# Optimization experiments

Hardware: AMD Instinct MI355X
Metric: run time of the kernel (lower is better)

The kernel has to match this reference:

```python
import jax, jax.numpy as jnp
import numpy as np

NLAT_IN, NLON_IN = 360, 720
NLAT_OUT, NLON_OUT = 180, 360
KERNEL_SIZE = 3
THETA_CUTOFF = KERNEL_SIZE * np.pi / NLAT_IN  # default theta_cutoff
B, C = 2, 64


def _cc_lats_weights(n):
    # Clenshaw-Curtis quadrature on [-1,1] (torch-harmonics 'equiangular' grid);
    # latitudes (colatitude) = arccos(nodes) = pi*k/(n-1) in [0, pi].
    N = n - 1
    theta = np.pi * np.arange(n) / N
    w = np.ones(n)
    for j in range(1, N // 2 + 1):
        b = 1.0 if 2 * j == N else 2.0
        w -= b * np.cos(2.0 * j * theta) / (4.0 * j * j - 1.0)
    w *= 2.0 / N
    w[0] *= 0.5
    w[-1] *= 0.5
    return theta, w


def _precompute_psi():
    # Mirrors _precompute_convolution_tensor + _compute_support_vals_isotropic.
    d_theta = THETA_CUTOFF / KERNEL_SIZE
    lats_in, _ = _cc_lats_weights(NLAT_IN)
    lats_out, _ = _cc_lats_weights(NLAT_OUT)
    phis = np.linspace(0.0, 2.0 * np.pi, NLON_IN)
    alpha = -lats_in[None, :, None].astype(np.float32)   # [1, H, 1]
    beta = phis[None, None, :].astype(np.float32)        # [1, 1, W]
    gamma = lats_out[:, None, None].astype(np.float32)   # [T, 1, 1]
    z = np.cos(alpha) * np.cos(gamma) - np.cos(beta) * np.sin(alpha) * np.sin(gamma)
    with np.errstate(invalid="ignore"):
        theta = np.arccos(z)  # [T, H, W]; nan where |z|>1 (excluded by mask, as in torch)
    segs, lats, lons, vals = [], [], [], []
    for ik in range(KERNEL_SIZE):
        itheta = ik * d_theta
        with np.errstate(invalid="ignore"):
            mask = (np.abs(theta - itheta) < d_theta) & (theta < THETA_CUTOFF)
        t_idx, h_idx, w_idx = np.nonzero(mask)
        segs.append(ik * NLAT_OUT + t_idx)  # fused (kernel, nlat_out) segment id
        lats.append(h_idx)
        lons.append(w_idx)
        vals.append(1.0 - np.abs(theta[mask] - itheta) / d_theta)
    return (np.concatenate(segs).astype(np.int32),
            np.concatenate(lats).astype(np.int32),
            np.concatenate(lons).astype(np.int32),
            np.concatenate(vals).astype(np.float32))


def setup_inputs() -> dict:
    key = jax.random.key(0)
    x = jax.random.normal(key, (B, C, NLAT_IN, NLON_IN), dtype=jnp.float32)
    _, wgl = _cc_lats_weights(NLAT_IN)
    quad_weights = jnp.asarray(2.0 * np.pi * wgl[:, None] / NLON_IN, dtype=jnp.float32)
    seg, lat, lon, val = _precompute_psi()
    return {"x": x, "quad_weights": quad_weights,
            "psi_seg": jnp.asarray(seg), "psi_lat": jnp.asarray(lat),
            "psi_lon": jnp.asarray(lon), "psi_val": jnp.asarray(val)}


def reference(x, quad_weights, psi_seg, psi_lat, psi_lon, psi_val):
    # out[b,c,k,t,p] = sum_{(k,t,h,w) in psi} val * qw[h] * x[b,c,h,(w-(p+1)*s) mod W]
    Bx, Cx, H, W = x.shape
    scale = W // NLON_OUT  # longitudinal shift per output longitude (torch.roll step)
    xw = (quad_weights * x).reshape(Bx * Cx, H, W)  # [BC, H, W]
    num_seg = KERNEL_SIZE * NLAT_OUT

    def step(carry, p):
        cols = (psi_lon - (p + 1) * scale) % W                 # rolled longitude per nnz
        g = xw[:, psi_lat, cols] * psi_val                     # [BC, nnz] gather + scale
        out_p = jax.ops.segment_sum(g.T, psi_seg, num_segments=num_seg)  # [K*T, BC]
        return carry, out_p

    _, ys = jax.lax.scan(step, None, jnp.arange(NLON_OUT))     # [P, K*T, BC]
    out = ys.transpose(2, 1, 0).reshape(Bx, Cx, KERNEL_SIZE, NLAT_OUT, NLON_OUT)
    return out
```

## Files before the change

kernel.cpp:

```cpp
#include <hip/hip_runtime.h>


#define NLAT_IN  360
#define NLON_IN  720
#define NLAT_OUT 180
#define NLON_OUT 360
#define KSIZE    3
#define NSEG     (KSIZE * NLAT_OUT)
#define CHW      (NLAT_IN * NLON_IN)
#define BCTOT    128
#define G        4
#define NBCG     (BCTOT / G)
#define MAXR     2
#define PH       10
#define NTHREADS 256
#define SLOTS    432
#define MIRROR   (SLOTS - NLON_OUT)
#define ROWB     (SLOTS * 16)

typedef float v2f __attribute__((ext_vector_type(2)));

__device__ __forceinline__ void PKF(v2f& a, v2f x, v2f c) {
    asm("v_pk_fma_f32 %0, %1, %2, %0" : "+v"(a) : "v"(x), "v"(c));
}


__global__ void prep1_kernel(const int* __restrict__ seg, const int* __restrict__ lat,
                             const float* __restrict__ val, int nnz,
                             int* __restrict__ ptrh, int* __restrict__ hbase,
                             int* __restrict__ hlast, int* __restrict__ flags) {
    int idx = blockIdx.x * blockDim.x + threadIdx.x;
    if (idx >= NSEG * PH) return;
    int s = idx / PH, j = idx - s * PH;
    int lo = 0, hi = nnz;
    while (lo < hi) { int m = (lo + hi) >> 1; if (seg[m] < s) lo = m + 1; else hi = m; }
    int e0 = lo;
    lo = e0; hi = nnz;
    while (lo < hi) { int m = (lo + hi) >> 1; if (seg[m] < s + 1) lo = m + 1; else hi = m; }
    int e1 = lo;
    if (e0 >= e1) {
        ptrh[idx] = e0; flags[idx] = 0;
        if (j == 0) { hbase[s] = 1 << 28; hlast[s] = -(1 << 28); }
        return;
    }
    int hb = lat[e0];
    if (j == 0) { hbase[s] = hb; hlast[s] = lat[e1 - 1]; }
    int a;
    { int tg = hb + j; lo = e0; hi = e1;
      while (lo < hi) { int m = (lo + hi) >> 1; if (lat[m] < tg) lo = m + 1; else hi = m; }
      a = lo; }
    ptrh[idx] = a;
    int f = 0;
    if (j < PH - 1) {
        int tg = hb + j + 1; lo = a; hi = e1;
        while (lo < hi) { int m = (lo + hi) >> 1; if (lat[m] < tg) lo = m + 1; else hi = m; }
        int b = lo;
        if (b - a == NLON_IN) {
            float v0 = val[a], v1 = val[a + 240], v2 = val[a + 480];
            float d = fmaxf(fabsf(v0 - v1), fmaxf(fabsf(v0 - v2), fabsf(v1 - v2)));
            f = (d < 1e-5f) ? 1 : 0;
        }
    }
    flags[idx] = f;
}

__global__ void span_kernel(const int* __restrict__ hbase, const int* __restrict__ hlast,
                            int* __restrict__ hbU, int* __restrict__ hlU) {
    int t = blockIdx.x * blockDim.x + threadIdx.x;
    if (t >= NLAT_OUT) return;
    int lo = 1 << 28, hi = -(1 << 28);
#pragma unroll
    for (int k = 0; k < KSIZE; ++k) {
        lo = min(lo, hbase[k * NLAT_OUT + t]);
        hi = max(hi, hlast[k * NLAT_OUT + t]);
    }
    hbU[t] = lo; hlU[t] = hi;
}

__global__ void cf_kernel(const int* __restrict__ lat, const float* __restrict__ val,
                          const float* __restrict__ qw, int nnz, float* __restrict__ cfb) {
    int e = blockIdx.x * blockDim.x + threadIdx.x;
    if (e < nnz) cfb[e] = val[e] * qw[lat[e]];
}

__global__ void runs_kernel(const int* __restrict__ lon, const int* __restrict__ ptrh,
                            const int* __restrict__ flags,
                            int* __restrict__ runcnt, uint2* __restrict__ runslab) {
    const int idx  = blockIdx.x * 4 + (threadIdx.x >> 6);
    if (idx >= NSEG * PH) return;
    const int lane = threadIdx.x & 63;
    const int j = idx % PH;
    int runbase = 0;
    if (j < PH - 1) {
        const int a = ptrh[idx], b = ptrh[idx + 1];
        if (b > a && !flags[idx]) {
            for (int c = a; c < b; c += 64) {
                const int e = c + lane;
                const bool active = e < b;
                const int w   = active ? lon[e] : 0;
                const int wm1 = (active && e > a) ? lon[e - 1] : -99;
                const bool isStart = active && (lane == 0 || w != wm1 + 1);
                const unsigned long long mask = __ballot(isStart);
                if (isStart) {
                    const int cnt = min(64, b - c);
                    unsigned long long hv = (mask >> lane) >> 1;
                    const int len = hv ? __ffsll((long long)hv) : (cnt - lane);
                    const int cidx = __popcll(mask & ((1ull << lane) - 1ull));
                    const int s0 = ((w >> 1) + NLON_OUT - 1) % NLON_OUT;
                    runslab[a + runbase + cidx] = make_uint2(
                        (unsigned)e, (unsigned)(s0 | ((w & 1) << 9) | (len << 11)));
                }
                runbase += __popcll(mask);
            }
        }
    }
    if (lane == 0) runcnt[idx] = runbase;
}


__global__ __launch_bounds__(NTHREADS) void disco_kernel(
    const float* __restrict__ x,
    const float* __restrict__ cfb,
    const uint2* __restrict__ runslab,
    const int*   __restrict__ runcnt,
    const int*   __restrict__ ptrh,
    const int*   __restrict__ hbase,
    const int*   __restrict__ flags,
    const int*   __restrict__ hbU,
    const int*   __restrict__ hlU,
    float*       __restrict__ out)
{
    __shared__ float4 smem4[MAXR * 2 * SLOTS];
    float4 (*ldsx)[SLOTS] = (float4(*)[SLOTS])smem4;
    v2f    (*accbuf)[6]   = (v2f(*)[6])smem4;

    const int tid      = threadIdx.x;
    const int lane     = tid & 63;
    const int wpair    = tid >> 7;
    const int pairlane = tid & 127;
    const int pid      = (pairlane < 120) ? pairlane : pairlane - 120;
    const int p0       = 3 * pid;
    const int bc0      = blockIdx.x * G;
    const int ty       = blockIdx.y;
    const int t        = (ty & 1) ? (NLAT_OUT - 1 - (ty >> 1)) : (ty >> 1);

    const int rlo = hbU[t], rhi = hlU[t];
    const int hbK0 = hbase[t];
    const int hbK1 = hbase[NLAT_OUT + t];
    const int hbK2 = hbase[2 * NLAT_OUT + t];

    v2f acc[KSIZE][6] = {};
    const char* lb = (const char*)smem4;

    float2 sv0[4], sv1[4], sv2[4];
    const float* xb = x + (size_t)bc0 * CHW;

#define LOADW(R0)                                                              \
    {                                                                          \
        {   const int idx_ = tid;                                              \
            const int rr_ = idx_ >= 360;                                       \
            const int m_  = idx_ - 360 * rr_;                                  \
            const int row_ = min((R0) + rr_, rhi);                             \
            const float* xr_ = xb + (size_t)row_ * NLON_IN + 2 * m_;           \
            sv0[0] = *(const float2*)(xr_);                                    \
            sv0[1] = *(const float2*)(xr_ + CHW);                              \
            sv0[2] = *(const float2*)(xr_ + 2 * CHW);                          \
            sv0[3] = *(const float2*)(xr_ + 3 * CHW);                          \
        }                                                                      \
        {   const int idx_ = tid + 256;                                        \
            const int rr_ = idx_ >= 360;                                       \
            const int m_  = idx_ - 360 * rr_;                                  \
            const int row_ = min((R0) + rr_, rhi);                             \
            const float* xr_ = xb + (size_t)row_ * NLON_IN + 2 * m_;           \
            sv1[0] = *(const float2*)(xr_);                                    \
            sv1[1] = *(const float2*)(xr_ + CHW);                              \
            sv1[2] = *(const float2*)(xr_ + 2 * CHW);                          \
            sv1[3] = *(const float2*)(xr_ + 3 * CHW);                          \
        }                                                                      \
        if (tid < 208) {                                                       \
            const int m_  = tid + 512 - 360;                                   \
            const int row_ = min((R0) + 1, rhi);                               \
            const float* xr_ = xb + (size_t)row_ * NLON_IN + 2 * m_;           \
            sv2[0] = *(const float2*)(xr_);                                    \
            sv2[1] = *(const float2*)(xr_ + CHW);                              \
            sv2[2] = *(const float2*)(xr_ + 2 * CHW);                          \
            sv2[3] = *(const float2*)(xr_ + 3 * CHW);                          \
        }                                                                      \
    }

#define WRITEW()                                                               \
    {                                                                          \
        {   const int idx_ = tid;                                              \
            const int rr_ = idx_ >= 360;                                       \
            const int m_  = idx_ - 360 * rr_;                                  \
            const float4 ev_ = {sv0[0].x, sv0[1].x, sv0[2].x, sv0[3].x};       \
            const float4 ov_ = {sv0[0].y, sv0[1].y, sv0[2].y, sv0[3].y};       \
            ldsx[2 * rr_ + 0][m_] = ev_;                                       \
            ldsx[2 * rr_ + 1][m_] = ov_;                                       \
            if (m_ < MIRROR) {                                                 \
                ldsx[2 * rr_ + 0][NLON_OUT + m_] = ev_;                        \
                ldsx[2 * rr_ + 1][NLON_OUT + m_] = ov_;                        \
            }                                                                  \
        }                                                                      \
        {   const int idx_ = tid + 256;                                        \
            const int rr_ = idx_ >= 360;                                       \
            const int m_  = idx_ - 360 * rr_;                                  \
            const float4 ev_ = {sv1[0].x, sv1[1].x, sv1[2].x, sv1[3].x};       \
            const float4 ov_ = {sv1[0].y, sv1[1].y, sv1[2].y, sv1[3].y};       \
            ldsx[2 * rr_ + 0][m_] = ev_;                                       \
            ldsx[2 * rr_ + 1][m_] = ov_;                                       \
            if (m_ < MIRROR) {                                                 \
                ldsx[2 * rr_ + 0][NLON_OUT + m_] = ev_;                        \
                ldsx[2 * rr_ + 1][NLON_OUT + m_] = ov_;                        \
            }                                                                  \
        }                                                                      \
        if (tid < 208) {                                                       \
            const int m_ = tid + 512 - 360;                                    \
            const float4 ev_ = {sv2[0].x, sv2[1].x, sv2[2].x, sv2[3].x};       \
            const float4 ov_ = {sv2[0].y, sv2[1].y, sv2[2].y, sv2[3].y};       \
            ldsx[2][m_] = ev_;                                                 \
            ldsx[3][m_] = ov_;                                                 \
            if (m_ < MIRROR) {                                                 \
                ldsx[2][NLON_OUT + m_] = ev_;                                  \
                ldsx[3][NLON_OUT + m_] = ov_;                                  \
            }                                                                  \
        }                                                                      \
    }

#define PROCRUNS(ASTART, RC, RP0, ACC)                                         \
    for (int rr = 0; rr < (RC); ++rr) {                                        \
        const uint2 R = runslab[(ASTART) + rr];                                \
        const int e0_ = __builtin_amdgcn_readfirstlane((int)R.x);              \
        const int y_  = __builtin_amdgcn_readfirstlane((int)R.y);              \
        const int s0A = y_ & 511;                                              \
        const int odd = (y_ >> 9) & 1;                                         \
        const int len = y_ >> 11;                                              \
        int qA = s0A - p0 - 2; qA += (qA >> 31) & NLON_OUT;                    \
        const char* baseA = lb + (size_t)((RP0) + odd) * ROWB + ((size_t)qA << 4); \
        const char* baseB = lb + (size_t)((RP0) + (odd ^ 1)) * ROWB            \
                               + ((size_t)(qA + odd) << 4);                    \
        const float* cfp = cfb + e0_;                                          \
        int i = 0;                                                             \
        if (len >= 8) {                                                        \
            v2f A0l = *(const v2f*)(baseA +  0), A0h = *(const v2f*)(baseA +  8); \
            v2f A1l = *(const v2f*)(baseA + 16), A1h = *(const v2f*)(baseA + 24); \
            v2f A2l = *(const v2f*)(baseA + 32), A2h = *(const v2f*)(baseA + 40); \
            v2f B0l = *(const v2f*)(baseB +  0), B0h = *(const v2f*)(baseB +  8); \
            v2f B1l = *(const v2f*)(baseB + 16), B1h = *(const v2f*)(baseB + 24); \
            v2f B2l = *(const v2f*)(baseB + 32), B2h = *(const v2f*)(baseB + 40); \
            v2f A3l, A3h, B3l, B3h;                                            \
            const char* ldA = baseA + 48;                                      \
            const char* ldB = baseB + 48;                                      \
            for (; i + 8 <= len; i += 8) {                                     \
                float cs; v2f c;                                               \
                A3l = *(const v2f*)(ldA); A3h = *(const v2f*)(ldA + 8); ldA += 16; \
                cs = cfp[i + 0]; c = (v2f){cs, cs};                            \
                PKF(ACC[4], A0l, c); PKF(ACC[5], A0h, c);                      \
                PKF(ACC[2], A1l, c); PKF(ACC[3], A1h, c);                      \
                PKF(ACC[0], A2l, c); PKF(ACC[1], A2h, c);                      \
                B3l = *(const v2f*)(ldB); B3h = *(const v2f*)(ldB + 8); ldB += 16; \
                cs = cfp[i + 1]; c = (v2f){cs, cs};                            \
                PKF(ACC[4], B0l, c); PKF(ACC[5], B0h, c);                      \
                PKF(ACC[2], B1l, c); PKF(ACC[3], B1h, c);                      \
                PKF(ACC[0], B2l, c); PKF(ACC[1], B2h, c);                      \
                A0l = *(const v2f*)(ldA); A0h = *(const v2f*)(ldA + 8); ldA += 16; \
                cs = cfp[i + 2]; c = (v2f){cs, cs};                            \
                PKF(ACC[4], A1l, c); PKF(ACC[5], A1h, c);                      \
                PKF(ACC[2], A2l, c); PKF(ACC[3], A2h, c);                      \
                PKF(ACC[0], A3l, c); PKF(ACC[1], A3h, c);                      \
                B0l = *(const v2f*)(ldB); B0h = *(const v2f*)(ldB + 8); ldB += 16; \
                cs = cfp[i + 3]; c = (v2f){cs, cs};                            \
                PKF(ACC[4], B1l, c); PKF(ACC[5], B1h, c);                      \
                PKF(ACC[2], B2l, c); PKF(ACC[3], B2h, c);                      \
                PKF(ACC[0], B3l, c); PKF(ACC[1], B3h, c);                      \
                A1l = *(const v2f*)(ldA); A1h = *(const v2f*)(ldA + 8); ldA += 16; \
                cs = cfp[i + 4]; c = (v2f){cs, cs};                            \
                PKF(ACC[4], A2l, c); PKF(ACC[5], A2h, c);                      \
                PKF(ACC[2], A3l, c); PKF(ACC[3], A3h, c);                      \
                PKF(ACC[0], A0l, c); PKF(ACC[1], A0h, c);                      \
                B1l = *(const v2f*)(ldB); B1h = *(const v2f*)(ldB + 8); ldB += 16; \
                cs = cfp[i + 5]; c = (v2f){cs, cs};                            \
                PKF(ACC[4], B2l, c); PKF(ACC[5], B2h, c);                      \
                PKF(ACC[2], B3l, c); PKF(ACC[3], B3h, c);                      \
                PKF(ACC[0], B0l, c); PKF(ACC[1], B0h, c);                      \
                A2l = *(const v2f*)(ldA); A2h = *(const v2f*)(ldA + 8); ldA += 16; \
                cs = cfp[i + 6]; c = (v2f){cs, cs};                            \
                PKF(ACC[4], A3l, c); PKF(ACC[5], A3h, c);                      \
                PKF(ACC[2], A0l, c); PKF(ACC[3], A0h, c);                      \
                PKF(ACC[0], A1l, c); PKF(ACC[1], A1h, c);                      \
                B2l = *(const v2f*)(ldB); B2h = *(const v2f*)(ldB + 8); ldB += 16; \
                cs = cfp[i + 7]; c = (v2f){cs, cs};                            \
                PKF(ACC[4], B3l, c); PKF(ACC[5], B3h, c);                      \
                PKF(ACC[2], B0l, c); PKF(ACC[3], B0h, c);                      \
                PKF(ACC[0], B1l, c); PKF(ACC[1], B1h, c);                      \
            }                                                                  \
        }                                                                      \
        for (; i < len; ++i) {                                                 \
            const int m_ = i >> 1;                                             \
            const char* bp = (i & 1) ? (baseB + ((size_t)m_ << 4))             \
                                     : (baseA + ((size_t)m_ << 4));            \
            const float cs = cfp[i]; const v2f c = (v2f){cs, cs};              \
            const v2f w0l = *(const v2f*)(bp +  0), w0h = *(const v2f*)(bp +  8); \
            const v2f w1l = *(const v2f*)(bp + 16), w1h = *(const v2f*)(bp + 24); \
            const v2f w2l = *(const v2f*)(bp + 32), w2h = *(const v2f*)(bp + 40); \
            PKF(ACC[4], w0l, c); PKF(ACC[5], w0h, c);                          \
            PKF(ACC[2], w1l, c); PKF(ACC[3], w1h, c);                          \
            PKF(ACC[0], w2l, c); PKF(ACC[1], w2h, c);                          \
        }                                                                      \
    }

    if (rlo <= rhi) {
        LOADW(rlo);
        for (int r0 = rlo; r0 <= rhi; r0 += MAXR) {
            const int rn = min(MAXR, rhi - r0 + 1);
            __syncthreads();
            WRITEW();
            if (r0 + MAXR <= rhi) LOADW(r0 + MAXR);
            __syncthreads();
            for (int r = 0; r < rn; ++r) {
                if ((r & 1) != wpair) continue;
                const int row = r0 + r;
                const int rp0 = r * 2;
                int aK[KSIZE], bK[KSIZE], fK[KSIZE], rcK[KSIZE];
                const int hbKs[KSIZE] = {hbK0, hbK1, hbK2};
#pragma unroll
                for (int k = 0; k < KSIZE; ++k) {
                    const int jk = row - hbKs[k];
                    const int ok = (jk >= 0) && (jk < PH - 1);
                    const int idxk = (k * NLAT_OUT + t) * PH + (ok ? jk : 0);
                    aK[k]  = ok ? ptrh[idxk] : 0;
                    bK[k]  = ok ? ptrh[idxk + 1] : 0;
                    fK[k]  = (ok && bK[k] > aK[k]) ? flags[idxk] : 0;
                    rcK[k] = (ok && bK[k] > aK[k] && !fK[k]) ? runcnt[idxk] : 0;
                }
                if (fK[0] | fK[1] | fK[2]) {
                    float4 v = {0.f, 0.f, 0.f, 0.f};
                    for (int m = lane; m < NLON_OUT; m += 64) {
                        const float4 u0 = ldsx[rp0][m], u1 = ldsx[rp0 + 1][m];
                        v.x += u0.x + u1.x; v.y += u0.y + u1.y;
                        v.z += u0.z + u1.z; v.w += u0.w + u1.w;
                    }
#pragma unroll
                    for (int o = 32; o >= 1; o >>= 1) {
                        v.x += __shfl_xor(v.x, o); v.y += __shfl_xor(v.y, o);
                        v.z += __shfl_xor(v.z, o); v.w += __shfl_xor(v.w, o);
                    }
#pragma unroll
                    for (int k = 0; k < KSIZE; ++k) {
                        if (fK[k]) {
                            const float cf = cfb[aK[k]];
                            acc[k][0].x = fmaf(cf, v.x, acc[k][0].x);
                            acc[k][0].y = fmaf(cf, v.y, acc[k][0].y);
                            acc[k][1].x = fmaf(cf, v.z, acc[k][1].x);
                            acc[k][1].y = fmaf(cf, v.w, acc[k][1].y);
                            acc[k][2].x = fmaf(cf, v.x, acc[k][2].x);
                            acc[k][2].y = fmaf(cf, v.y, acc[k][2].y);
                            acc[k][3].x = fmaf(cf, v.z, acc[k][3].x);
                            acc[k][3].y = fmaf(cf, v.w, acc[k][3].y);
                            acc[k][4].x = fmaf(cf, v.x, acc[k][4].x);
                            acc[k][4].y = fmaf(cf, v.y, acc[k][4].y);
                            acc[k][5].x = fmaf(cf, v.z, acc[k][5].x);
                            acc[k][5].y = fmaf(cf, v.w, acc[k][5].y);
                        }
                    }
                }
#pragma unroll
                for (int k = 0; k < KSIZE; ++k) {
                    if (rcK[k] > 0) { PROCRUNS(aK[k], rcK[k], rp0, acc[k]); }
                }
            }
        }
    }

    const size_t cs_ = (size_t)NSEG * NLON_OUT;
#pragma unroll
    for (int k = 0; k < KSIZE; ++k) {
        __syncthreads();
        if (wpair == 1 && pairlane < 120) {
            accbuf[pid][0] = acc[k][0]; accbuf[pid][1] = acc[k][1];
            accbuf[pid][2] = acc[k][2]; accbuf[pid][3] = acc[k][3];
            accbuf[pid][4] = acc[k][4]; accbuf[pid][5] = acc[k][5];
        }
        __syncthreads();
        if (wpair == 0 && pairlane < 120) {
            const v2f b0 = accbuf[pid][0], b1 = accbuf[pid][1];
            const v2f b2 = accbuf[pid][2], b3 = accbuf[pid][3];
            const v2f b4 = accbuf[pid][4], b5 = accbuf[pid][5];
            const v2f r0_ = acc[k][0] + b0, r1_ = acc[k][1] + b1;
            const v2f r2_ = acc[k][2] + b2, r3_ = acc[k][3] + b3;
            const v2f r4_ = acc[k][4] + b4, r5_ = acc[k][5] + b5;
            const size_t ob = ((size_t)bc0 * NSEG + k * NLAT_OUT + t) * NLON_OUT + p0;
            out[ob]              = r0_.x; out[ob + 1]              = r2_.x; out[ob + 2]              = r4_.x;
            out[ob + cs_]        = r0_.y; out[ob + cs_ + 1]        = r2_.y; out[ob + cs_ + 2]        = r4_.y;
            out[ob + 2 * cs_]    = r1_.x; out[ob + 2 * cs_ + 1]    = r3_.x; out[ob + 2 * cs_ + 2]    = r5_.x;
            out[ob + 3 * cs_]    = r1_.y; out[ob + 3 * cs_ + 1]    = r3_.y; out[ob + 3 * cs_ + 2]    = r5_.y;
        }
    }
#undef LOADW
#undef WRITEW
#undef PROCRUNS
}


__global__ void segptr_kernel(const int* __restrict__ seg, int nnz, int* __restrict__ ptr) {
    int s = blockIdx.x * blockDim.x + threadIdx.x;
    if (s > NSEG) return;
    if (s == NSEG) { ptr[NSEG] = nnz; return; }
    int lo = 0, hi = nnz;
    while (lo < hi) { int m = (lo + hi) >> 1; if (seg[m] < s) lo = m + 1; else hi = m; }
    ptr[s] = lo;
}

__global__ __launch_bounds__(384) void disco_simple_kernel(
    const float* __restrict__ x, const float* __restrict__ qw,
    const int* __restrict__ lat, const int* __restrict__ lon,
    const float* __restrict__ val, const int* __restrict__ ptr,
    float* __restrict__ out)
{
    const int p = threadIdx.x;
    if (p >= NLON_OUT) return;
    const int kt = blockIdx.x, bc0 = blockIdx.y * 8;
    const int e0 = ptr[kt], e1 = ptr[kt + 1];
    float acc[8];
#pragma unroll
    for (int g = 0; g < 8; ++g) acc[g] = 0.0f;
    const int pw = 2 * p + 2;
    const float* xb = x + (size_t)bc0 * CHW;
    for (int e = e0; e < e1; ++e) {
        const int h = lat[e], w = lon[e];
        const float cf = val[e] * qw[h];
        int col = w - pw; if (col < 0) col += NLON_IN;
        const float* src = xb + h * NLON_IN + col;
#pragma unroll
        for (int g = 0; g < 8; ++g) acc[g] = fmaf(cf, src[(size_t)g * CHW], acc[g]);
    }
    const size_t ob = ((size_t)bc0 * NSEG + kt) * NLON_OUT + p;
#pragma unroll
    for (int g = 0; g < 8; ++g) out[ob + (size_t)g * NSEG * NLON_OUT] = acc[g];
}


extern "C" void kernel_launch(void* const* d_in, const int* in_sizes, int n_in,
                              void* d_out, int out_size, void* d_ws, size_t ws_size,
                              hipStream_t stream)
{
    const float* x   = (const float*)d_in[0];
    const float* qw  = (const float*)d_in[1];
    const int*   seg = (const int*)  d_in[2];
    const int*   lat = (const int*)  d_in[3];
    const int*   lon = (const int*)  d_in[4];
    const float* val = (const float*)d_in[5];
    const int    nnz = in_sizes[2];
    const int    nnzpad = (nnz + 3) & ~3;

    char* w = (char*)d_ws;
    size_t off = 0;
    int* ptrh   = (int*)(w + off); off += (size_t)NSEG * PH * 4;
    int* hbase  = (int*)(w + off); off += NSEG * 4;
    int* hlast  = (int*)(w + off); off += NSEG * 4;
    int* flags  = (int*)(w + off); off += (size_t)NSEG * PH * 4;
    int* runcnt = (int*)(w + off); off += (size_t)NSEG * PH * 4;
    int* hbU    = (int*)(w + off); off += NLAT_OUT * 4;
    int* hlU    = (int*)(w + off); off += NLAT_OUT * 4;
    float* cfb  = (float*)(w + off); off += (size_t)nnzpad * 4;
    off = (off + 7) & ~(size_t)7;
    uint2* runslab = (uint2*)(w + off); off += (size_t)nnz * 8;

    if (ws_size < off) {
        int* ptr = (int*)d_ws;
        segptr_kernel<<<(NSEG + 1 + 255) / 256, 256, 0, stream>>>(seg, nnz, ptr);
        dim3 grid(NSEG, BCTOT / 8);
        disco_simple_kernel<<<grid, 384, 0, stream>>>(x, qw, lat, lon, val, ptr,
                                                      (float*)d_out);
        return;
    }

    prep1_kernel<<<(NSEG * PH + 255) / 256, 256, 0, stream>>>(seg, lat, val, nnz,
                                                              ptrh, hbase, hlast, flags);
    span_kernel<<<1, 256, 0, stream>>>(hbase, hlast, hbU, hlU);
    cf_kernel<<<(nnz + 255) / 256, 256, 0, stream>>>(lat, val, qw, nnz, cfb);
    runs_kernel<<<(NSEG * PH + 3) / 4, 256, 0, stream>>>(lon, ptrh, flags,
                                                         runcnt, runslab);

    dim3 grid(NBCG, NLAT_OUT);
    disco_kernel<<<grid, NTHREADS, 0, stream>>>(x, cfb, runslab, runcnt,
                                                ptrh, hbase, flags, hbU, hlU,
                                                (float*)d_out);
}
```

Baseline: 166.1 us.

## Tile disco blocks over two adjacent output latitudes per kernel index

Each block now handles one kernel index and two neighbouring output latitudes, instead of one latitude with all three kernel indices. The grid gains a z dimension for the kernel index, and the span_kernel launch is removed because row ranges now come directly from hbase/hlast. The LDS slot count drops from 432 to 400, which shrinks shared memory and may allow more blocks per CU. The row-to-wave assignment also changes from parity to a direct match, and neighbouring latitudes share row ranges, so input reuse and the number of rows loaded per block change.

```diff
diff --git a/kernel.cpp b/kernel.cpp
--- a/kernel.cpp
+++ b/kernel.cpp
@@ -14,7 +14,7 @@
 #define MAXR     2
 #define PH       10
 #define NTHREADS 256
-#define SLOTS    432
+#define SLOTS    400
 #define MIRROR   (SLOTS - NLON_OUT)
 #define ROWB     (SLOTS * 16)
 
@@ -62,19 +62,6 @@
         }
     }
     flags[idx] = f;
-}
-
-__global__ void span_kernel(const int* __restrict__ hbase, const int* __restrict__ hlast,
-                            int* __restrict__ hbU, int* __restrict__ hlU) {
-    int t = blockIdx.x * blockDim.x + threadIdx.x;
-    if (t >= NLAT_OUT) return;
-    int lo = 1 << 28, hi = -(1 << 28);
-#pragma unroll
-    for (int k = 0; k < KSIZE; ++k) {
-        lo = min(lo, hbase[k * NLAT_OUT + t]);
-        hi = max(hi, hlast[k * NLAT_OUT + t]);
-    }
-    hbU[t] = lo; hlU[t] = hi;
 }
 
 __global__ void cf_kernel(const int* __restrict__ lat, const float* __restrict__ val,
@@ -125,14 +112,12 @@
     const int*   __restrict__ runcnt,
     const int*   __restrict__ ptrh,
     const int*   __restrict__ hbase,
+    const int*   __restrict__ hlast,
     const int*   __restrict__ flags,
-    const int*   __restrict__ hbU,
-    const int*   __restrict__ hlU,
     float*       __restrict__ out)
 {
-    __shared__ float4 smem4[MAXR * 2 * SLOTS];
-    float4 (*ldsx)[SLOTS] = (float4(*)[SLOTS])smem4;
-    v2f    (*accbuf)[6]   = (v2f(*)[6])smem4;
+    __shared__ float4 ldsx[MAXR * 2][SLOTS];
+    v2f (*accbuf)[6] = (v2f(*)[6])&ldsx[0][0];
 
     const int tid      = threadIdx.x;
     const int lane     = tid & 63;
@@ -142,15 +127,17 @@
     const int p0       = 3 * pid;
     const int bc0      = blockIdx.x * G;
     const int ty       = blockIdx.y;
-    const int t        = (ty & 1) ? (NLAT_OUT - 1 - (ty >> 1)) : (ty >> 1);
-
-    const int rlo = hbU[t], rhi = hlU[t];
-    const int hbK0 = hbase[t];
-    const int hbK1 = hbase[NLAT_OUT + t];
-    const int hbK2 = hbase[2 * NLAT_OUT + t];
-
-    v2f acc[KSIZE][6] = {};
-    const char* lb = (const char*)smem4;
+    const int tp       = (ty & 1) ? (89 - (ty >> 1)) : (ty >> 1);
+    const int t0       = 2 * tp;
+    const int sBase    = blockIdx.z * NLAT_OUT + t0;
+
+    const int hbT0 = hbase[sBase],     hlT0 = hlast[sBase];
+    const int hbT1 = hbase[sBase + 1], hlT1 = hlast[sBase + 1];
+    const int rlo = min(hbT0, hbT1);
+    const int rhi = max(hlT0, hlT1);
+
+    v2f acc[2][6] = {};
+    const char* lb = (const char*)&ldsx[0][0];
 
     float2 sv0[4], sv1[4], sv2[4];
     const float* xb = x + (size_t)bc0 * CHW;
@@ -255,44 +242,44 @@
                 float cs; v2f c;                                               \
                 A3l = *(const v2f*)(ldA); A3h = *(const v2f*)(ldA + 8); ldA += 16; \
                 cs = cfp[i + 0]; c = (v2f){cs, cs};                            \
-                PKF(ACC[4], A0l, c); PKF(ACC[5], A0h, c);                      \
-                PKF(ACC[2], A1l, c); PKF(ACC[3], A1h, c);                      \
-                PKF(ACC[0], A2l, c); PKF(ACC[1], A2h, c);                      \
+                PKF((ACC)[4], A0l, c); PKF((ACC)[5], A0h, c);                  \
+                PKF((ACC)[2], A1l, c); PKF((ACC)[3], A1h, c);                  \
+                PKF((ACC)[0], A2l, c); PKF((ACC)[1], A2h, c);                  \
                 B3l = *(const v2f*)(ldB); B3h = *(const v2f*)(ldB + 8); ldB += 16; \
                 cs = cfp[i + 1]; c = (v2f){cs, cs};                            \
-                PKF(ACC[4], B0l, c); PKF(ACC[5], B0h, c);                      \
-                PKF(ACC[2], B1l, c); PKF(ACC[3], B1h, c);                      \
-                PKF(ACC[0], B2l, c); PKF(ACC[1], B2h, c);                      \
+                PKF((ACC)[4], B0l, c); PKF((ACC)[5], B0h, c);                  \
+                PKF((ACC)[2], B1l, c); PKF((ACC)[3], B1h, c);                  \
+                PKF((ACC)[0], B2l, c); PKF((ACC)[1], B2h, c);                  \
                 A0l = *(const v2f*)(ldA); A0h = *(const v2f*)(ldA + 8); ldA += 16; \
                 cs = cfp[i + 2]; c = (v2f){cs, cs};                            \
-                PKF(ACC[4], A1l, c); PKF(ACC[5], A1h, c);                      \
-                PKF(ACC[2], A2l, c); PKF(ACC[3], A2h, c);                      \
-                PKF(ACC[0], A3l, c); PKF(ACC[1], A3h, c);                      \
+                PKF((ACC)[4], A1l, c); PKF((ACC)[5], A1h, c);                  \
+                PKF((ACC)[2], A2l, c); PKF((ACC)[3], A2h, c);                  \
+                PKF((ACC)[0], A3l, c); PKF((ACC)[1], A3h, c);                  \
                 B0l = *(const v2f*)(ldB); B0h = *(const v2f*)(ldB + 8); ldB += 16; \
                 cs = cfp[i + 3]; c = (v2f){cs, cs};                            \
-                PKF(ACC[4], B1l, c); PKF(ACC[5], B1h, c);                      \
-                PKF(ACC[2], B2l, c); PKF(ACC[3], B2h, c);                      \
-                PKF(ACC[0], B3l, c); PKF(ACC[1], B3h, c);                      \
+                PKF((ACC)[4], B1l, c); PKF((ACC)[5], B1h, c);                  \
+                PKF((ACC)[2], B2l, c); PKF((ACC)[3], B2h, c);                  \
+                PKF((ACC)[0], B3l, c); PKF((ACC)[1], B3h, c);                  \
                 A1l = *(const v2f*)(ldA); A1h = *(const v2f*)(ldA + 8); ldA += 16; \
                 cs = cfp[i + 4]; c = (v2f){cs, cs};                            \
-                PKF(ACC[4], A2l, c); PKF(ACC[5], A2h, c);                      \
-                PKF(ACC[2], A3l, c); PKF(ACC[3], A3h, c);                      \
-                PKF(ACC[0], A0l, c); PKF(ACC[1], A0h, c);                      \
+                PKF((ACC)[4], A2l, c); PKF((ACC)[5], A2h, c);                  \
+                PKF((ACC)[2], A3l, c); PKF((ACC)[3], A3h, c);                  \
+                PKF((ACC)[0], A0l, c); PKF((ACC)[1], A0h, c);                  \
                 B1l = *(const v2f*)(ldB); B1h = *(const v2f*)(ldB + 8); ldB += 16; \
                 cs = cfp[i + 5]; c = (v2f){cs, cs};                            \
-                PKF(ACC[4], B2l, c); PKF(ACC[5], B2h, c);                      \
-                PKF(ACC[2], B3l, c); PKF(ACC[3], B3h, c);                      \
-                PKF(ACC[0], B0l, c); PKF(ACC[1], B0h, c);                      \
+                PKF((ACC)[4], B2l, c); PKF((ACC)[5], B2h, c);                  \
+                PKF((ACC)[2], B3l, c); PKF((ACC)[3], B3h, c);                  \
+                PKF((ACC)[0], B0l, c); PKF((ACC)[1], B0h, c);                  \
                 A2l = *(const v2f*)(ldA); A2h = *(const v2f*)(ldA + 8); ldA += 16; \
                 cs = cfp[i + 6]; c = (v2f){cs, cs};                            \
-                PKF(ACC[4], A3l, c); PKF(ACC[5], A3h, c);                      \
-                PKF(ACC[2], A0l, c); PKF(ACC[3], A0h, c);                      \
-                PKF(ACC[0], A1l, c); PKF(ACC[1], A1h, c);                      \
+                PKF((ACC)[4], A3l, c); PKF((ACC)[5], A3h, c);                  \
+                PKF((ACC)[2], A0l, c); PKF((ACC)[3], A0h, c);                  \
+                PKF((ACC)[0], A1l, c); PKF((ACC)[1], A1h, c);                  \
                 B2l = *(const v2f*)(ldB); B2h = *(const v2f*)(ldB + 8); ldB += 16; \
                 cs = cfp[i + 7]; c = (v2f){cs, cs};                            \
-                PKF(ACC[4], B3l, c); PKF(ACC[5], B3h, c);                      \
-                PKF(ACC[2], B0l, c); PKF(ACC[3], B0h, c);                      \
-                PKF(ACC[0], B1l, c); PKF(ACC[1], B1h, c);                      \
+                PKF((ACC)[4], B3l, c); PKF((ACC)[5], B3h, c);                  \
+                PKF((ACC)[2], B0l, c); PKF((ACC)[3], B0h, c);                  \
+                PKF((ACC)[0], B1l, c); PKF((ACC)[1], B1h, c);                  \
             }                                                                  \
         }                                                                      \
         for (; i < len; ++i) {                                                 \
@@ -303,13 +290,14 @@
             const v2f w0l = *(const v2f*)(bp +  0), w0h = *(const v2f*)(bp +  8); \
             const v2f w1l = *(const v2f*)(bp + 16), w1h = *(const v2f*)(bp + 24); \
             const v2f w2l = *(const v2f*)(bp + 32), w2h = *(const v2f*)(bp + 40); \
-            PKF(ACC[4], w0l, c); PKF(ACC[5], w0h, c);                          \
-            PKF(ACC[2], w1l, c); PKF(ACC[3], w1h, c);                          \
-            PKF(ACC[0], w2l, c); PKF(ACC[1], w2h, c);                          \
+            PKF((ACC)[4], w0l, c); PKF((ACC)[5], w0h, c);                      \
+            PKF((ACC)[2], w1l, c); PKF((ACC)[3], w1h, c);                      \
+            PKF((ACC)[0], w2l, c); PKF((ACC)[1], w2h, c);                      \
         }                                                                      \
     }
 
     if (rlo <= rhi) {
+        const int hbT[2] = {hbT0, hbT1};
         LOADW(rlo);
         for (int r0 = rlo; r0 <= rhi; r0 += MAXR) {
             const int rn = min(MAXR, rhi - r0 + 1);
@@ -318,22 +306,21 @@
             if (r0 + MAXR <= rhi) LOADW(r0 + MAXR);
             __syncthreads();
             for (int r = 0; r < rn; ++r) {
-                if ((r & 1) != wpair) continue;
+                if (r != wpair) continue;
                 const int row = r0 + r;
                 const int rp0 = r * 2;
-                int aK[KSIZE], bK[KSIZE], fK[KSIZE], rcK[KSIZE];
-                const int hbKs[KSIZE] = {hbK0, hbK1, hbK2};
-#pragma unroll
-                for (int k = 0; k < KSIZE; ++k) {
-                    const int jk = row - hbKs[k];
+                int aT[2], bT[2], fT[2], rcT[2];
+#pragma unroll
+                for (int tt = 0; tt < 2; ++tt) {
+                    const int jk = row - hbT[tt];
                     const int ok = (jk >= 0) && (jk < PH - 1);
-                    const int idxk = (k * NLAT_OUT + t) * PH + (ok ? jk : 0);
-                    aK[k]  = ok ? ptrh[idxk] : 0;
-                    bK[k]  = ok ? ptrh[idxk + 1] : 0;
-                    fK[k]  = (ok && bK[k] > aK[k]) ? flags[idxk] : 0;
-                    rcK[k] = (ok && bK[k] > aK[k] && !fK[k]) ? runcnt[idxk] : 0;
+                    const int idxk = (sBase + tt) * PH + (ok ? jk : 0);
+                    aT[tt]  = ok ? ptrh[idxk] : 0;
+                    bT[tt]  = ok ? ptrh[idxk + 1] : 0;
+                    fT[tt]  = (ok && bT[tt] > aT[tt]) ? flags[idxk] : 0;
+                    rcT[tt] = (ok && bT[tt] > aT[tt] && !fT[tt]) ? runcnt[idxk] : 0;
                 }
-                if (fK[0] | fK[1] | fK[2]) {
+                if (fT[0] | fT[1]) {
                     float4 v = {0.f, 0.f, 0.f, 0.f};
                     for (int m = lane; m < NLON_OUT; m += 64) {
                         const float4 u0 = ldsx[rp0][m], u1 = ldsx[rp0 + 1][m];
@@ -346,27 +333,27 @@
                         v.z += __shfl_xor(v.z, o); v.w += __shfl_xor(v.w, o);
                     }
 #pragma unroll
-                    for (int k = 0; k < KSIZE; ++k) {
-                        if (fK[k]) {
-                            const float cf = cfb[aK[k]];
-                            acc[k][0].x = fmaf(cf, v.x, acc[k][0].x);
-                            acc[k][0].y = fmaf(cf, v.y, acc[k][0].y);
-                            acc[k][1].x = fmaf(cf, v.z, acc[k][1].x);
-                            acc[k][1].y = fmaf(cf, v.w, acc[k][1].y);
-                            acc[k][2].x = fmaf(cf, v.x, acc[k][2].x);
-                            acc[k][2].y = fmaf(cf, v.y, acc[k][2].y);
-                            acc[k][3].x = fmaf(cf, v.z, acc[k][3].x);
-                            acc[k][3].y = fmaf(cf, v.w, acc[k][3].y);
-                            acc[k][4].x = fmaf(cf, v.x, acc[k][4].x);
-                            acc[k][4].y = fmaf(cf, v.y, acc[k][4].y);
-                            acc[k][5].x = fmaf(cf, v.z, acc[k][5].x);
-                            acc[k][5].y = fmaf(cf, v.w, acc[k][5].y);
+                    for (int tt = 0; tt < 2; ++tt) {
+                        if (fT[tt]) {
+                            const float cf = cfb[aT[tt]];
+                            acc[tt][0].x = fmaf(cf, v.x, acc[tt][0].x);
+                            acc[tt][0].y = fmaf(cf, v.y, acc[tt][0].y);
+                            acc[tt][1].x = fmaf(cf, v.z, acc[tt][1].x);
+                            acc[tt][1].y = fmaf(cf, v.w, acc[tt][1].y);
+                            acc[tt][2].x = fmaf(cf, v.x, acc[tt][2].x);
+                            acc[tt][2].y = fmaf(cf, v.y, acc[tt][2].y);
+                            acc[tt][3].x = fmaf(cf, v.z, acc[tt][3].x);
+                            acc[tt][3].y = fmaf(cf, v.w, acc[tt][3].y);
+                            acc[tt][4].x = fmaf(cf, v.x, acc[tt][4].x);
+                            acc[tt][4].y = fmaf(cf, v.y, acc[tt][4].y);
+                            acc[tt][5].x = fmaf(cf, v.z, acc[tt][5].x);
+                            acc[tt][5].y = fmaf(cf, v.w, acc[tt][5].y);
                         }
                     }
                 }
 #pragma unroll
-                for (int k = 0; k < KSIZE; ++k) {
-                    if (rcK[k] > 0) { PROCRUNS(aK[k], rcK[k], rp0, acc[k]); }
+                for (int tt = 0; tt < 2; ++tt) {
+                    if (rcT[tt] > 0) { PROCRUNS(aT[tt], rcT[tt], rp0, acc[tt]); }
                 }
             }
         }
@@ -374,22 +361,22 @@
 
     const size_t cs_ = (size_t)NSEG * NLON_OUT;
 #pragma unroll
-    for (int k = 0; k < KSIZE; ++k) {
+    for (int tt = 0; tt < 2; ++tt) {
         __syncthreads();
         if (wpair == 1 && pairlane < 120) {
-            accbuf[pid][0] = acc[k][0]; accbuf[pid][1] = acc[k][1];
-            accbuf[pid][2] = acc[k][2]; accbuf[pid][3] = acc[k][3];
-            accbuf[pid][4] = acc[k][4]; accbuf[pid][5] = acc[k][5];
+            accbuf[pid][0] = acc[tt][0]; accbuf[pid][1] = acc[tt][1];
+            accbuf[pid][2] = acc[tt][2]; accbuf[pid][3] = acc[tt][3];
+            accbuf[pid][4] = acc[tt][4]; accbuf[pid][5] = acc[tt][5];
         }
         __syncthreads();
         if (wpair == 0 && pairlane < 120) {
-            const v2f b0 = accbuf[pid][0], b1 = accbuf[pid][1];
-            const v2f b2 = accbuf[pid][2], b3 = accbuf[pid][3];
-            const v2f b4 = accbuf[pid][4], b5 = accbuf[pid][5];
-            const v2f r0_ = acc[k][0] + b0, r1_ = acc[k][1] + b1;
-            const v2f r2_ = acc[k][2] + b2, r3_ = acc[k][3] + b3;
-            const v2f r4_ = acc[k][4] + b4, r5_ = acc[k][5] + b5;
-            const size_t ob = ((size_t)bc0 * NSEG + k * NLAT_OUT + t) * NLON_OUT + p0;
+            const v2f r0_ = acc[tt][0] + accbuf[pid][0];
+            const v2f r1_ = acc[tt][1] + accbuf[pid][1];
+            const v2f r2_ = acc[tt][2] + accbuf[pid][2];
+            const v2f r3_ = acc[tt][3] + accbuf[pid][3];
+            const v2f r4_ = acc[tt][4] + accbuf[pid][4];
+            const v2f r5_ = acc[tt][5] + accbuf[pid][5];
+            const size_t ob = ((size_t)bc0 * NSEG + sBase + tt) * NLON_OUT + p0;
             out[ob]              = r0_.x; out[ob + 1]              = r2_.x; out[ob + 2]              = r4_.x;
             out[ob + cs_]        = r0_.y; out[ob + cs_ + 1]        = r2_.y; out[ob + cs_ + 2]        = r4_.y;
             out[ob + 2 * cs_]    = r1_.x; out[ob + 2 * cs_ + 1]    = r3_.x; out[ob + 2 * cs_ + 2]    = r5_.x;
@@ -460,8 +447,6 @@
     int* hlast  = (int*)(w + off); off += NSEG * 4;
     int* flags  = (int*)(w + off); off += (size_t)NSEG * PH * 4;
     int* runcnt = (int*)(w + off); off += (size_t)NSEG * PH * 4;
-    int* hbU    = (int*)(w + off); off += NLAT_OUT * 4;
-    int* hlU    = (int*)(w + off); off += NLAT_OUT * 4;
     float* cfb  = (float*)(w + off); off += (size_t)nnzpad * 4;
     off = (off + 7) & ~(size_t)7;
     uint2* runslab = (uint2*)(w + off); off += (size_t)nnz * 8;
@@ -477,13 +462,12 @@
 
     prep1_kernel<<<(NSEG * PH + 255) / 256, 256, 0, stream>>>(seg, lat, val, nnz,
                                                               ptrh, hbase, hlast, flags);
-    span_kernel<<<1, 256, 0, stream>>>(hbase, hlast, hbU, hlU);
     cf_kernel<<<(nnz + 255) / 256, 256, 0, stream>>>(lat, val, qw, nnz, cfb);
     runs_kernel<<<(NSEG * PH + 3) / 4, 256, 0, stream>>>(lon, ptrh, flags,
                                                          runcnt, runslab);
 
-    dim3 grid(NBCG, NLAT_OUT);
+    dim3 grid(NBCG, NLAT_OUT / 2, KSIZE);
     disco_kernel<<<grid, NTHREADS, 0, stream>>>(x, cfb, runslab, runcnt,
-                                                ptrh, hbase, flags, hbU, hlU,
+                                                ptrh, hbase, hlast, flags,
                                                 (float*)d_out);
 }
```

After: 191.6 us. 15.4% more time.
